# Kernel optimization log

Hardware: AMD Instinct MI355X
Metric: run time of the kernel (lower is better)

The kernel has to match this reference:

```python
import jax, jax.numpy as jnp
import numpy as np

ROPE_THETA = 10000.0

def _rope(t):
    # t: (B, S, H, D) -- rotate-half RoPE over last dim
    B, S, H, D = t.shape
    inv_freq = 1.0 / (ROPE_THETA ** (jnp.arange(0, D, 2, dtype=jnp.float32) / D))  # (D/2,)
    ang = jnp.arange(S, dtype=jnp.float32)[:, None] * inv_freq[None, :]            # (S, D/2)
    cos = jnp.concatenate([jnp.cos(ang), jnp.cos(ang)], axis=-1)[None, :, None, :] # (1,S,1,D)
    sin = jnp.concatenate([jnp.sin(ang), jnp.sin(ang)], axis=-1)[None, :, None, :]
    t1, t2 = jnp.split(t, 2, axis=-1)
    rot = jnp.concatenate([-t2, t1], axis=-1)
    return t * cos.astype(t.dtype) + rot * sin.astype(t.dtype)

def setup_inputs() -> dict:
    key = jax.random.key(0)
    kx, kq, kk, kv, ko = jax.random.split(key, 5)
    B, S, DIM = 2, 2048, 2048
    x = jax.random.normal(kx, (B, S, DIM), dtype=jnp.float32)
    mask = jnp.tril(jnp.ones((S, S), dtype=bool))[None, None, :, :]  # causal (1,1,S,S)
    scale = DIM ** -0.5
    wq = jax.random.normal(kq, (DIM, DIM), dtype=jnp.float32) * scale
    wk = jax.random.normal(kk, (DIM, DIM), dtype=jnp.float32) * scale
    wv = jax.random.normal(kv, (DIM, DIM), dtype=jnp.float32) * scale
    wo = jax.random.normal(ko, (DIM, DIM), dtype=jnp.float32) * scale
    return {"x": x, "mask": mask, "wq": wq, "wk": wk, "wv": wv, "wo": wo}

def reference(x, mask, wq, wk, wv, wo):
    B, S, DIM = x.shape
    H = 16
    D = DIM // H
    scale = D ** -0.5
    # nn.Linear: y = x @ W.T
    q = (x @ wq.T).reshape(B, S, H, D)
    k = (x @ wk.T).reshape(B, S, H, D)
    v = (x @ wv.T).reshape(B, S, H, D)
    q = _rope(q)
    k = _rope(k)
    scores = jnp.einsum('bqhd,bkhd->bhqk', q, k) * scale
    scores = jnp.where(mask, scores, -jnp.inf)
    attn = jax.nn.softmax(scores, axis=-1)
    out = jnp.einsum('bhqk,bkhd->bqhd', attn, v).reshape(B, S, DIM)
    return out @ wo.T
```

## Files before the change

kernel.cpp:

```cpp
#include <hip/hip_runtime.h>
#include <cstdint>

typedef unsigned short u16;
typedef uint32_t u32;
typedef __attribute__((ext_vector_type(8))) short bf16x8;
typedef __attribute__((ext_vector_type(4))) float f32x4;
typedef __attribute__((ext_vector_type(16))) float f32x16;

#define DIM_ 2048
#define S_   2048
#define B_   2
#define H_   16
#define HD_  128
#define M_   (B_ * S_)

__device__ __forceinline__ u16 f2b(float f) {
  union { float f; uint32_t u; } v; v.f = f;
  uint32_t u = v.u;
  return (u16)((u + 0x7FFFu + ((u >> 16) & 1u)) >> 16);
}
__device__ __forceinline__ float b2f(u16 h) {
  union { uint32_t u; float f; } v; v.u = ((uint32_t)h) << 16;
  return v.f;
}

__device__ __forceinline__ u32 cvtpk(float lo, float hi) {
  u32 r;
  asm("v_cvt_pk_bf16_f32 %0, %1, %2" : "=v"(r) : "v"(lo), "v"(hi));
  return r;
}

typedef __attribute__((address_space(3))) u16 lds_u16_t;
typedef __attribute__((address_space(1))) const u16 glob_u16_t;

__device__ __forceinline__ void gload16(const u16* g, u16* l) {
  __builtin_amdgcn_global_load_lds((glob_u16_t*)g, (lds_u16_t*)l, 16, 0, 0);
}
#define GLD0(SRC, DST) \
  __builtin_amdgcn_global_load_lds((glob_u16_t*)(SRC), (lds_u16_t*)(DST), 16, 0, 0)

__global__ void convert5_kernel(const float* __restrict__ x, const float* __restrict__ wq,
                                const float* __restrict__ wk, const float* __restrict__ wv,
                                const float* __restrict__ wo, u16* __restrict__ xb,
                                u16* __restrict__ wqb, u16* __restrict__ wkb,
                                u16* __restrict__ wvb, u16* __restrict__ wob) {
  const float* src;
  u16* dst;
  int n;
  switch (blockIdx.y) {
    case 0: src = x;  dst = xb;  n = M_ * DIM_;   break;
    case 1: src = wq; dst = wqb; n = DIM_ * DIM_; break;
    case 2: src = wk; dst = wkb; n = DIM_ * DIM_; break;
    case 3: src = wv; dst = wvb; n = DIM_ * DIM_; break;
    default: src = wo; dst = wob; n = DIM_ * DIM_; break;
  }
  int i = (blockIdx.x * blockDim.x + threadIdx.x) * 4;
  const int stride = gridDim.x * blockDim.x * 4;
  for (; i < n; i += stride) {
    float4 v = *reinterpret_cast<const float4*>(src + i);
    uint64_t p = (uint64_t)f2b(v.x) | ((uint64_t)f2b(v.y) << 16) |
                 ((uint64_t)f2b(v.z) << 32) | ((uint64_t)f2b(v.w) << 48);
    *reinterpret_cast<uint64_t*>(dst + i) = p;
  }
}

__global__ void rope_table_kernel(float* __restrict__ cosT, float* __restrict__ sinT) {
  int i = blockIdx.x * blockDim.x + threadIdx.x;
  if (i >= S_ * 64) return;
  int s = i >> 6, d = i & 63;
  float inv = powf(10000.0f, -(float)d * (1.0f / 64.0f));
  float ang = (float)s * inv;
  cosT[i] = cosf(ang);
  sinT[i] = sinf(ang);
}

__global__ void rope_apply_kernel(u16* __restrict__ qb, u16* __restrict__ kb,
                                  const float* __restrict__ cosT,
                                  const float* __restrict__ sinT) {
  u16* buf = blockIdx.y ? kb : qb;
  int i = blockIdx.x * blockDim.x + threadIdx.x;
  if (i >= B_ * S_ * H_ * 64) return;
  int d = i & 63;
  int h = (i >> 6) & (H_ - 1);
  int row = i >> 10;
  int s = row & (S_ - 1);
  u16* p = buf + (size_t)row * DIM_ + h * HD_ + d;
  float t1 = b2f(p[0]);
  float t2 = b2f(p[64]);
  float c = cosT[s * 64 + d];
  float sn = sinT[s * 64 + d];
  p[0]  = f2b(t1 * c - t2 * sn);
  p[64] = f2b(t2 * c + t1 * sn);
}

#define NT_ 32

#define LDA(DST, BASE)                                                         \
  _Pragma("unroll") for (int mi = 0; mi < 8; ++mi)                             \
      DST[mi] = *(const bf16x8*)((BASE) + mi * 1024);
#define LDB(DST, BASE)                                                         \
  _Pragma("unroll") for (int ni = 0; ni < NF_; ++ni)                           \
      DST[ni] = *(const bf16x8*)((BASE) + ni * 1024);

#define MFMA_KS(AV, BV)                                                        \
  _Pragma("unroll") for (int mi = 0; mi < 8; ++mi)                             \
    _Pragma("unroll") for (int ni = 0; ni < NF_; ++ni)                         \
        acc[mi][ni] = __builtin_amdgcn_mfma_f32_16x16x32_bf16(                 \
            AV[mi], BV[ni], acc[mi][ni], 0, 0, 0);

#define STAGE(BUF, OFFU) do {                                                  \
    _Pragma("unroll") for (int s = 0; s < ASW_; ++s)                           \
      GLD0(sA + goff + (OFFU) + s * (64 * DIM_),                               \
           lds + (BUF) * BUFSZ_ + s * 4096 + w * 512);                         \
    _Pragma("unroll") for (int s = 0; s < BSW_; ++s)                           \
      GLD0(sB + goff + (OFFU) + s * (64 * DIM_),                               \
           lds + (BUF) * BUFSZ_ + 16384 + s * 4096 + w * 512);                 \
  } while (0)

#define VMC_N() do {                                                           \
    if (ASW_ + BSW_ == 8) asm volatile("s_waitcnt vmcnt(8)" ::: "memory");     \
    else                  asm volatile("s_waitcnt vmcnt(6)" ::: "memory");     \
  } while (0)

#define TILE_N(BUF, NBUF, OFFU) do {                                           \
    LDA(a1, pAk1[BUF]); LDB(b1, pBk1[BUF]);                            \
    __builtin_amdgcn_sched_barrier(0);                                         \
    __builtin_amdgcn_s_setprio(1);                                             \
    MFMA_KS(a0, b0);                                                  \
    __builtin_amdgcn_s_setprio(0);                                             \
    asm volatile("s_waitcnt lgkmcnt(0)" ::: "memory");                         \
    __builtin_amdgcn_sched_barrier(0);                                         \
    __builtin_amdgcn_s_barrier();                                      \
    STAGE(BUF, OFFU);                                                          \
    __builtin_amdgcn_sched_barrier(0);                                         \
    VMC_N();                                                                   \
    __builtin_amdgcn_sched_barrier(0);                                         \
    __builtin_amdgcn_s_barrier();                                      \
    LDA(a0, pAk0[NBUF]); LDB(b0, pBk0[NBUF]);                          \
    __builtin_amdgcn_sched_barrier(0);                                         \
    __builtin_amdgcn_s_setprio(1);                                             \
    MFMA_KS(a1, b1);                                                  \
    __builtin_amdgcn_s_setprio(0);                                             \
  } while (0)

#define TILE_P(BUF, NBUF) do {                                   \
    LDA(a1, pAk1[BUF]); LDB(b1, pBk1[BUF]);                                    \
    __builtin_amdgcn_sched_barrier(0);                                         \
    __builtin_amdgcn_s_setprio(1);                                             \
    MFMA_KS(a0, b0);                                                           \
    __builtin_amdgcn_s_setprio(0);                                             \
    asm volatile("s_waitcnt lgkmcnt(0)" ::: "memory");                         \
    __builtin_amdgcn_sched_barrier(0);                                         \
    asm volatile("s_waitcnt vmcnt(0)" ::: "memory");                           \
    __builtin_amdgcn_sched_barrier(0);                                         \
    __builtin_amdgcn_s_barrier();                                              \
    LDA(a0, pAk0[NBUF]); LDB(b0, pBk0[NBUF]);                                  \
    __builtin_amdgcn_sched_barrier(0);                                         \
    __builtin_amdgcn_s_setprio(1);                                             \
    MFMA_KS(a1, b1);                                                           \
    __builtin_amdgcn_s_setprio(0);                                             \
  } while (0)

#define TILE_L(BUF) do {                                         \
    LDA(a1, pAk1[BUF]); LDB(b1, pBk1[BUF]);                                    \
    __builtin_amdgcn_sched_barrier(0);                                         \
    MFMA_KS(a0, b0);                                                           \
    MFMA_KS(a1, b1);                                                           \
  } while (0)

#define GEMM_V2_BODY(BN_)                                                      \
  constexpr int NF_ = (BN_) / 64;                 \
  constexpr int ASW_ = 4;                   \
  constexpr int BSW_ = (BN_) / 64;                         \
  constexpr int BUFSZ_ = 16384 + (BN_) * 64;               \
  const int tid = threadIdx.x;                                                 \
  const int lane = tid & 63;                                                   \
  const int w = tid >> 6;                                                      \
  const int wm = w >> 2, wn = w & 3;                                           \
  const int l15 = lane & 15, lg = lane >> 4;                                   \
    \
  const int goff = (w * 8 + (lane >> 3)) * DIM_ + ((lane & 7) ^ (lane >> 3)) * 8; \
     \
  const int x7 = l15 & 7;                                                      \
  const int lr0 = l15 * 64 + ((lg ^ x7) * 8);                                  \
  const int lr1 = l15 * 64 + (((4 | lg) ^ x7) * 8);                            \
  const u16* pAk0[2] = {lds + wm * 8192 + lr0, lds + BUFSZ_ + wm * 8192 + lr0};\
  const u16* pAk1[2] = {lds + wm * 8192 + lr1, lds + BUFSZ_ + wm * 8192 + lr1};\
  const u16* pBk0[2] = {lds + 16384 + wn * ((BN_)*16) + lr0,                   \
                        lds + BUFSZ_ + 16384 + wn * ((BN_)*16) + lr0};         \
  const u16* pBk1[2] = {lds + 16384 + wn * ((BN_)*16) + lr1,                   \
                        lds + BUFSZ_ + 16384 + wn * ((BN_)*16) + lr1};         \
  f32x4 acc[8][NF_];                                                           \
  _Pragma("unroll") for (int i = 0; i < 8; ++i)                                \
    _Pragma("unroll") for (int j = 0; j < NF_; ++j)                            \
        acc[i][j] = (f32x4){0.f, 0.f, 0.f, 0.f};                               \
  bf16x8 a0[8], a1[8], b0[NF_], b1[NF_];                                       \
             \
  STAGE(0, 0);                                                                 \
  STAGE(1, 64);                                                                \
  __builtin_amdgcn_sched_barrier(0);                                           \
  VMC_N();                                                                     \
  __builtin_amdgcn_sched_barrier(0);                                           \
  __builtin_amdgcn_s_barrier();                                                \
  LDA(a0, pAk0[0]); LDB(b0, pBk0[0]);                                          \
  for (int t = 0; t < NT_ - 2; t += 2) {                                       \
    TILE_N(0, 1, 128);                                                         \
    TILE_N(1, 0, 192);                                                         \
    sA += 128; sB += 128;                                                      \
  }                                                                            \
  TILE_P(0, 1);                                                                \
  TILE_L(1);

__global__ __launch_bounds__(512, 2) void gemm256_qkv_kernel(
    const u16* __restrict__ xb, const u16* __restrict__ wqb, const u16* __restrict__ wkb,
    const u16* __restrict__ wvb, u16* __restrict__ qb, u16* __restrict__ kb,
    u16* __restrict__ vb) {
  __shared__ __align__(16) u16 lds[65536];

  const int bid = blockIdx.x;
  const int logical = (bid & 7) * 48 + (bid >> 3);
  const int mt = logical / 24;
  const int rem = logical % 24;
  const int z = rem >> 3;
  const int nt = rem & 7;
  const u16* Wm = (z == 0) ? wqb : (z == 1) ? wkb : wvb;
  u16* out = (z == 0) ? qb : (z == 1) ? kb : vb;

  const u16* sA = xb + (size_t)(mt * 256) * DIM_;
  const u16* sB = Wm + (size_t)(nt * 256) * DIM_;

  GEMM_V2_BODY(256)

#pragma unroll
  for (int mi = 0; mi < 8; ++mi)
#pragma unroll
    for (int ni = 0; ni < 4; ++ni) {
      const int row = mt * 256 + wm * 128 + mi * 16 + lg * 4;
      const int col = nt * 256 + wn * 64 + ni * 16 + l15;
#pragma unroll
      for (int r = 0; r < 4; ++r)
        out[(size_t)(row + r) * DIM_ + col] = f2b(acc[mi][ni][r]);
    }
}

__global__ __launch_bounds__(512, 2) void gemm_out_v2_kernel(const u16* __restrict__ A,
                                                             const u16* __restrict__ W,
                                                             float* __restrict__ Cf) {
  __shared__ __align__(16) u16 lds[49152];
  const int bid = blockIdx.x;
  const int logical = (bid & 7) * 32 + (bid >> 3);
  const int mt = logical >> 4;
  const int nt = logical & 15;

  const u16* sA = A + (size_t)(mt * 256) * DIM_;
  const u16* sB = W + (size_t)(nt * 128) * DIM_;

  GEMM_V2_BODY(128)

#pragma unroll
  for (int mi = 0; mi < 8; ++mi)
#pragma unroll
    for (int ni = 0; ni < 2; ++ni) {
      const int row = mt * 256 + wm * 128 + mi * 16 + lg * 4;
      const int col = nt * 128 + wn * 32 + ni * 16 + l15;
#pragma unroll
      for (int r = 0; r < 4; ++r)
        Cf[(size_t)(row + r) * DIM_ + col] = acc[mi][ni][r];
    }
}

#define CEXP 0.12751744f

__global__ __launch_bounds__(256, 2) void attn_kernel(const u16* __restrict__ q,
                                                      const u16* __restrict__ k,
                                                      const u16* __restrict__ v,
                                                      u16* __restrict__ ao) {
  __shared__ __align__(16) u16 smem[17408];
  u16* kTl = smem;
  u16* vTl = smem + 8192;

  const int qt   = blockIdx.z ? (int)blockIdx.x : (int)(gridDim.x - 1 - blockIdx.x);
  const int head = blockIdx.y;
  const int b    = blockIdx.z;
  const int t = threadIdx.x;
  const int lane = t & 63;
  const int w = t >> 6;
  const int l31 = lane & 31;
  const int hi = lane >> 5;
  const int kxor = (lane & 7) << 3;
  const int qrow0 = qt * 128 + w * 32;
  const size_t bS = (size_t)b * S_;

  bf16x8 qf[8];
  {
    const u16* qrow = q + (bS + qrow0 + l31) * DIM_ + head * HD_;
#pragma unroll
    for (int st = 0; st < 8; ++st)
      qf[st] = *(const bf16x8*)(qrow + st * 16 + hi * 8);
  }

  f32x16 accO[4];
#pragma unroll
  for (int db = 0; db < 4; ++db)
#pragma unroll
    for (int r = 0; r < 16; ++r) accO[db][r] = 0.f;
  float m = -1e30f, l = 0.f;

  const int tmax_w = 2 * qt + (w >> 1);
  const int ttend = 2 * qt + 1;

  for (int tt = 0; tt <= ttend; ++tt) {
    __syncthreads();

    bf16x8 vv[4];
#pragma unroll
    for (int p = 0; p < 4; ++p) {
      const int dchunk = p * 4 + w;
      vv[p] = *(const bf16x8*)(v + (bS + tt * 64 + lane) * DIM_ + head * HD_ + dchunk * 8);
    }
#pragma unroll
    for (int p = 0; p < 4; ++p) {
      const int cb = p * 256 + t;
      const int cid = p * 256 + w * 64 + lane;
      const int kr = cid >> 4;
      const int cg = (cid & 15) ^ (kr & 7);
      gload16(k + (bS + tt * 64 + kr) * DIM_ + head * HD_ + cg * 8,
              kTl + (p * 256 + w * 64) * 8);
    }
#pragma unroll
    for (int p = 0; p < 4; ++p) {
      const int dchunk = p * 4 + w;
#pragma unroll
      for (int j = 0; j < 8; ++j) {
        const int d = dchunk * 8 + j;
        vTl[d * 64 + (lane ^ ((d & 7) << 3))] = (u16)vv[p][j];
      }
    }
    __syncthreads();

    if (tt <= tmax_w) {
      f32x16 sA, sB;
#pragma unroll
      for (int r = 0; r < 16; ++r) { sA[r] = 0.f; sB[r] = 0.f; }
      __builtin_amdgcn_s_setprio(1);
#pragma unroll
      for (int st = 0; st < 8; ++st) {
        const int dc = st * 16 + hi * 8;
        bf16x8 k0 = *(const bf16x8*)(kTl + l31 * 128 + (dc ^ kxor));
        bf16x8 k1 = *(const bf16x8*)(kTl + (32 + l31) * 128 + (dc ^ kxor));
        sA = __builtin_amdgcn_mfma_f32_32x32x16_bf16(k0, qf[st], sA, 0, 0, 0);
        sB = __builtin_amdgcn_mfma_f32_32x32x16_bf16(k1, qf[st], sB, 0, 0, 0);
      }
      __builtin_amdgcn_s_setprio(0);

      const int qg = qrow0 + l31;
      if (tt * 64 + 63 > qrow0) {
        const int kb = tt * 64 + 4 * hi;
#pragma unroll
        for (int r = 0; r < 16; ++r) {
          const int kg = kb + (r & 3) + 8 * (r >> 2);
          sA[r] = (kg <= qg) ? sA[r] : -1e30f;
          sB[r] = (kg + 32 <= qg) ? sB[r] : -1e30f;
        }
      }

      float mx[8];
#pragma unroll
      for (int i = 0; i < 8; ++i)
        mx[i] = fmaxf(fmaxf(sA[i], sA[i + 8]), fmaxf(sB[i], sB[i + 8]));
#pragma unroll
      for (int i = 0; i < 4; ++i) mx[i] = fmaxf(mx[i], mx[i + 4]);
      float pm = fmaxf(fmaxf(mx[0], mx[1]), fmaxf(mx[2], mx[3]));
      pm = fmaxf(pm, __shfl_xor(pm, 32));
      const float mN = fmaxf(m, pm);
      if (!__all(pm - m <= 90.5f)) {
        const float osc = exp2f((m - mN) * CEXP);
        l *= osc;
#pragma unroll
        for (int db = 0; db < 4; ++db)
#pragma unroll
          for (int r = 0; r < 16; ++r) accO[db][r] *= osc;
        m = mN;
      }
      const float mc = m * CEXP;
      float lsv[4] = {0.f, 0.f, 0.f, 0.f};
#pragma unroll
      for (int r = 0; r < 16; ++r) {
        const float pa = exp2f(__builtin_fmaf(sA[r], CEXP, -mc));
        const float pb = exp2f(__builtin_fmaf(sB[r], CEXP, -mc));
        sA[r] = pa; sB[r] = pb;
        lsv[r & 3] += pa + pb;
      }
      float ls = (lsv[0] + lsv[1]) + (lsv[2] + lsv[3]);
      ls += __shfl_xor(ls, 32);
      l += ls;

#define PV_STEP(ARR, R0, ST2)                                                      \
      {                                                                            \
        u32 a0 = cvtpk(ARR[(R0) + 0], ARR[(R0) + 1]);                              \
        u32 a1 = cvtpk(ARR[(R0) + 2], ARR[(R0) + 3]);                              \
        u32 b0 = cvtpk(ARR[(R0) + 4], ARR[(R0) + 5]);                              \
        u32 b1 = cvtpk(ARR[(R0) + 6], ARR[(R0) + 7]);                              \
        asm("v_permlane32_swap_b32 %0, %1" : "+v"(a0), "+v"(b0));                  \
        asm("v_permlane32_swap_b32 %0, %1" : "+v"(a1), "+v"(b1));                  \
        union { u32 uu[4]; bf16x8 v8; } pf;                                        \
        pf.uu[0] = a0; pf.uu[1] = a1; pf.uu[2] = b0; pf.uu[3] = b1;                \
        const int ko = (ST2) * 16 + hi * 8;                                        \
        __builtin_amdgcn_s_setprio(1);                                             \
        _Pragma("unroll")                                                          \
        for (int db = 0; db < 4; ++db) {                                           \
          const int dr = db * 32 + l31;                                            \
          bf16x8 vf = *(const bf16x8*)(vTl + dr * 64 + (ko ^ kxor));               \
          accO[db] =                                                               \
              __builtin_amdgcn_mfma_f32_32x32x16_bf16(vf, pf.v8, accO[db], 0, 0, 0); \
        }                                                                          \
        __builtin_amdgcn_s_setprio(0);                                             \
      }
      PV_STEP(sA, 0, 0)
      PV_STEP(sA, 8, 1)
      PV_STEP(sB, 0, 2)
      PV_STEP(sB, 8, 3)
#undef PV_STEP
    }
  }

  __syncthreads();
  const float linv = 1.0f / l;
  u16* oT = smem + w * 4352;
#pragma unroll
  for (int db = 0; db < 4; ++db)
#pragma unroll
    for (int q4 = 0; q4 < 4; ++q4) {
      const int dbase = db * 32 + q4 * 8 + hi * 4;
      const u32 lo = cvtpk(accO[db][q4 * 4 + 0] * linv, accO[db][q4 * 4 + 1] * linv);
      const u32 hiw = cvtpk(accO[db][q4 * 4 + 2] * linv, accO[db][q4 * 4 + 3] * linv);
      *(u32*)(oT + l31 * 136 + dbase) = lo;
      *(u32*)(oT + l31 * 136 + dbase + 2) = hiw;
    }
  __syncthreads();
#pragma unroll
  for (int i = 0; i < 8; ++i) {
    const int cid = i * 64 + lane;
    const int qloc = cid >> 4;
    const int c = cid & 15;
    const bf16x8 val = *(const bf16x8*)(oT + qloc * 136 + c * 8);
    *(bf16x8*)(ao + (bS + qrow0 + qloc) * DIM_ + head * HD_ + c * 8) = val;
  }
}

extern "C" void kernel_launch(void* const* d_in, const int* in_sizes, int n_in,
                              void* d_out, int out_size, void* d_ws, size_t ws_size,
                              hipStream_t stream) {
  const float* x  = (const float*)d_in[0];
  const float* wq = (const float*)d_in[2];
  const float* wk = (const float*)d_in[3];
  const float* wv = (const float*)d_in[4];
  const float* wo = (const float*)d_in[5];

  char* ws = (char*)d_ws;
  size_t off = 0;
  auto carve = [&](size_t bytes) { char* p = ws + off; off += bytes; return p; };
  u16* xb   = (u16*)carve((size_t)M_ * DIM_ * 2);
  u16* wqb  = (u16*)carve((size_t)DIM_ * DIM_ * 2);
  u16* wkb  = (u16*)carve((size_t)DIM_ * DIM_ * 2);
  u16* wvb  = (u16*)carve((size_t)DIM_ * DIM_ * 2);
  u16* wob  = (u16*)carve((size_t)DIM_ * DIM_ * 2);
  u16* qb   = (u16*)carve((size_t)M_ * DIM_ * 2);
  u16* kb   = (u16*)carve((size_t)M_ * DIM_ * 2);
  u16* vb   = (u16*)carve((size_t)M_ * DIM_ * 2);
  u16* aob  = (u16*)carve((size_t)M_ * DIM_ * 2);
  float* cosT = (float*)carve((size_t)S_ * 64 * 4);
  float* sinT = (float*)carve((size_t)S_ * 64 * 4);
  if (off > ws_size) return;

  dim3 gc(1024, 5);
  convert5_kernel<<<gc, 256, 0, stream>>>(x, wq, wk, wv, wo, xb, wqb, wkb, wvb, wob);
  rope_table_kernel<<<512, 256, 0, stream>>>(cosT, sinT);

  gemm256_qkv_kernel<<<384, 512, 0, stream>>>(xb, wqb, wkb, wvb, qb, kb, vb);

  dim3 gr((B_ * S_ * H_ * 64) / 256, 2);
  rope_apply_kernel<<<gr, 256, 0, stream>>>(qb, kb, cosT, sinT);

  dim3 ga(S_ / 128, H_, B_);
  attn_kernel<<<ga, 256, 0, stream>>>(qb, kb, vb, aob);

  gemm_out_v2_kernel<<<256, 512, 0, stream>>>(aob, wob, (float*)d_out);
}
```

Measured before the change: 285.4 us.

## Double-buffer K/V tiles in attention and vectorize RoPE apply

The attention kernel now double-buffers its K and V shared-memory tiles. It issues the async K load and the V register load for the next tile before computing the current one, then writes V to the alternate buffer afterwards, so global loads overlap with MFMA work and one barrier per iteration is removed. Shared memory per block grows from about 34KB to 64KB, which may lower occupancy. Separately, the RoPE apply kernel now handles 8 bf16 elements per thread with 16-byte vector loads and stores instead of scalar accesses.

```diff
diff --git a/kernel.cpp b/kernel.cpp
--- a/kernel.cpp
+++ b/kernel.cpp
@@ -79,18 +79,30 @@
                                   const float* __restrict__ sinT) {
   u16* buf = blockIdx.y ? kb : qb;
   int i = blockIdx.x * blockDim.x + threadIdx.x;
-  if (i >= B_ * S_ * H_ * 64) return;
-  int d = i & 63;
-  int h = (i >> 6) & (H_ - 1);
-  int row = i >> 10;
-  int s = row & (S_ - 1);
-  u16* p = buf + (size_t)row * DIM_ + h * HD_ + d;
-  float t1 = b2f(p[0]);
-  float t2 = b2f(p[64]);
-  float c = cosT[s * 64 + d];
-  float sn = sinT[s * 64 + d];
-  p[0]  = f2b(t1 * c - t2 * sn);
-  p[64] = f2b(t2 * c + t1 * sn);
+  if (i >= B_ * S_ * H_ * 8) return;
+  const int c8 = i & 7;
+  const int h = (i >> 3) & (H_ - 1);
+  const int row = i >> 7;
+  const int s = row & (S_ - 1);
+  u16* p = buf + (size_t)row * DIM_ + h * HD_ + c8 * 8;
+  bf16x8 t1v = *(bf16x8*)p;
+  bf16x8 t2v = *(bf16x8*)(p + 64);
+  const float4 c0 = *(const float4*)(cosT + s * 64 + c8 * 8);
+  const float4 c1 = *(const float4*)(cosT + s * 64 + c8 * 8 + 4);
+  const float4 s0 = *(const float4*)(sinT + s * 64 + c8 * 8);
+  const float4 s1 = *(const float4*)(sinT + s * 64 + c8 * 8 + 4);
+  const float cc[8] = {c0.x, c0.y, c0.z, c0.w, c1.x, c1.y, c1.z, c1.w};
+  const float ss[8] = {s0.x, s0.y, s0.z, s0.w, s1.x, s1.y, s1.z, s1.w};
+  bf16x8 o1, o2;
+#pragma unroll
+  for (int j = 0; j < 8; ++j) {
+    const float t1 = b2f((u16)t1v[j]);
+    const float t2 = b2f((u16)t2v[j]);
+    o1[j] = (short)f2b(t1 * cc[j] - t2 * ss[j]);
+    o2[j] = (short)f2b(t2 * cc[j] + t1 * ss[j]);
+  }
+  *(bf16x8*)p = o1;
+  *(bf16x8*)(p + 64) = o2;
 }
 
 #define NT_ 32
@@ -169,18 +181,16 @@
   } while (0)
 
 #define GEMM_V2_BODY(BN_)                                                      \
-  constexpr int NF_ = (BN_) / 64;                 \
-  constexpr int ASW_ = 4;                   \
-  constexpr int BSW_ = (BN_) / 64;                         \
-  constexpr int BUFSZ_ = 16384 + (BN_) * 64;               \
+  constexpr int NF_ = (BN_) / 64;                                              \
+  constexpr int ASW_ = 4;                                                      \
+  constexpr int BSW_ = (BN_) / 64;                                             \
+  constexpr int BUFSZ_ = 16384 + (BN_) * 64;                                   \
   const int tid = threadIdx.x;                                                 \
   const int lane = tid & 63;                                                   \
   const int w = tid >> 6;                                                      \
   const int wm = w >> 2, wn = w & 3;                                           \
   const int l15 = lane & 15, lg = lane >> 4;                                   \
-    \
   const int goff = (w * 8 + (lane >> 3)) * DIM_ + ((lane & 7) ^ (lane >> 3)) * 8; \
-     \
   const int x7 = l15 & 7;                                                      \
   const int lr0 = l15 * 64 + ((lg ^ x7) * 8);                                  \
   const int lr1 = l15 * 64 + (((4 | lg) ^ x7) * 8);                            \
@@ -195,7 +205,6 @@
     _Pragma("unroll") for (int j = 0; j < NF_; ++j)                            \
         acc[i][j] = (f32x4){0.f, 0.f, 0.f, 0.f};                               \
   bf16x8 a0[8], a1[8], b0[NF_], b1[NF_];                                       \
-             \
   STAGE(0, 0);                                                                 \
   STAGE(1, 64);                                                                \
   __builtin_amdgcn_sched_barrier(0);                                           \
@@ -275,9 +284,9 @@
                                                       const u16* __restrict__ k,
                                                       const u16* __restrict__ v,
                                                       u16* __restrict__ ao) {
-  __shared__ __align__(16) u16 smem[17408];
+  __shared__ __align__(16) u16 smem[32768];
   u16* kTl = smem;
-  u16* vTl = smem + 8192;
+  u16* vTl = smem + 16384;
 
   const int qt   = blockIdx.z ? (int)blockIdx.x : (int)(gridDim.x - 1 - blockIdx.x);
   const int head = blockIdx.y;
@@ -309,36 +318,54 @@
   const int tmax_w = 2 * qt + (w >> 1);
   const int ttend = 2 * qt + 1;
 
-  for (int tt = 0; tt <= ttend; ++tt) {
-    __syncthreads();
-
-    bf16x8 vv[4];
+  bf16x8 vv[4];
+
+  auto stageK = [&](int buf, int tt) {
 #pragma unroll
     for (int p = 0; p < 4; ++p) {
-      const int dchunk = p * 4 + w;
-      vv[p] = *(const bf16x8*)(v + (bS + tt * 64 + lane) * DIM_ + head * HD_ + dchunk * 8);
-    }
-#pragma unroll
-    for (int p = 0; p < 4; ++p) {
-      const int cb = p * 256 + t;
       const int cid = p * 256 + w * 64 + lane;
       const int kr = cid >> 4;
       const int cg = (cid & 15) ^ (kr & 7);
       gload16(k + (bS + tt * 64 + kr) * DIM_ + head * HD_ + cg * 8,
-              kTl + (p * 256 + w * 64) * 8);
-    }
+              kTl + buf * 8192 + (p * 256 + w * 64) * 8);
+    }
+  };
+  auto loadV = [&](int tt) {
 #pragma unroll
     for (int p = 0; p < 4; ++p) {
       const int dchunk = p * 4 + w;
+      vv[p] = *(const bf16x8*)(v + (bS + tt * 64 + lane) * DIM_ + head * HD_ + dchunk * 8);
+    }
+  };
+  auto writeV = [&](int buf) {
+#pragma unroll
+    for (int p = 0; p < 4; ++p) {
+      const int dchunk = p * 4 + w;
 #pragma unroll
       for (int j = 0; j < 8; ++j) {
         const int d = dchunk * 8 + j;
-        vTl[d * 64 + (lane ^ ((d & 7) << 3))] = (u16)vv[p][j];
+        vTl[buf * 8192 + d * 64 + (lane ^ ((d & 7) << 3))] = (u16)vv[p][j];
       }
     }
-    __syncthreads();
+  };
+
+  stageK(0, 0);
+  loadV(0);
+  writeV(0);
+  __syncthreads();
+
+  for (int tt = 0; tt <= ttend; ++tt) {
+    const int cur = tt & 1;
+    const int alt = cur ^ 1;
+
+    if (tt + 1 <= ttend) {
+      stageK(alt, tt + 1);
+      loadV(tt + 1);
+    }
 
     if (tt <= tmax_w) {
+      const u16* kB = kTl + cur * 8192;
+      const u16* vB = vTl + cur * 8192;
       f32x16 sA, sB;
 #pragma unroll
       for (int r = 0; r < 16; ++r) { sA[r] = 0.f; sB[r] = 0.f; }
@@ -346,8 +373,8 @@
 #pragma unroll
       for (int st = 0; st < 8; ++st) {
         const int dc = st * 16 + hi * 8;
-        bf16x8 k0 = *(const bf16x8*)(kTl + l31 * 128 + (dc ^ kxor));
-        bf16x8 k1 = *(const bf16x8*)(kTl + (32 + l31) * 128 + (dc ^ kxor));
+        bf16x8 k0 = *(const bf16x8*)(kB + l31 * 128 + (dc ^ kxor));
+        bf16x8 k1 = *(const bf16x8*)(kB + (32 + l31) * 128 + (dc ^ kxor));
         sA = __builtin_amdgcn_mfma_f32_32x32x16_bf16(k0, qf[st], sA, 0, 0, 0);
         sB = __builtin_amdgcn_mfma_f32_32x32x16_bf16(k1, qf[st], sB, 0, 0, 0);
       }
@@ -410,7 +437,7 @@
         _Pragma("unroll")                                                          \
         for (int db = 0; db < 4; ++db) {                                           \
           const int dr = db * 32 + l31;                                            \
-          bf16x8 vf = *(const bf16x8*)(vTl + dr * 64 + (ko ^ kxor));               \
+          bf16x8 vf = *(const bf16x8*)(vB + dr * 64 + (ko ^ kxor));                \
           accO[db] =                                                               \
               __builtin_amdgcn_mfma_f32_32x32x16_bf16(vf, pf.v8, accO[db], 0, 0, 0); \
         }                                                                          \
@@ -422,9 +449,11 @@
       PV_STEP(sB, 8, 3)
 #undef PV_STEP
     }
+
+    if (tt + 1 <= ttend) writeV(alt);
+    __syncthreads();
   }
 
-  __syncthreads();
   const float linv = 1.0f / l;
   u16* oT = smem + w * 4352;
 #pragma unroll
@@ -479,7 +508,7 @@
 
   gemm256_qkv_kernel<<<384, 512, 0, stream>>>(xb, wqb, wkb, wvb, qb, kb, vb);
 
-  dim3 gr((B_ * S_ * H_ * 64) / 256, 2);
+  dim3 gr((B_ * S_ * H_ * 8) / 256, 2);
   rope_apply_kernel<<<gr, 256, 0, stream>>>(qb, kb, cosT, sinT);
 
   dim3 ga(S_ / 128, H_, B_);
```

Result: faster. 277.9 us (-2.6%).
